# Performance work log

Hardware: AMD Instinct MI355X
Metric: run time of the kernel (lower is better)

Reference implementation:

```python
import jax, jax.numpy as jnp
import numpy as np

B, T, N = 16, 1000, 100
ENC, VOCAB, EMB, HID, ATT, PROJ = 512, 10025, 640, 1024, 1024, 1024


def setup_inputs() -> dict:
    key = jax.random.key(0)
    ks = jax.random.split(key, 20)
    g = lambda k, shape, s=0.02: (jax.random.normal(k, shape) * s).astype(jnp.float32)
    inp = {
        "encoder_outputs": jax.random.normal(ks[0], (B, T, ENC), dtype=jnp.float32),
        "labels": jax.random.randint(ks[1], (B, N), 0, VOCAB),
        "enc_seq_len": jax.random.randint(ks[2], (B,), T // 2, T + 1),
        # parameters (torch layout: Linear weight [out, in])
        "embed_table": g(ks[3], (VOCAB, EMB)),
        "W_ih": g(ks[4], (4 * HID, EMB + ENC)),
        "W_hh": g(ks[5], (4 * HID, HID)),
        "b_ih": jnp.zeros((4 * HID,), jnp.float32),
        "b_hh": jnp.zeros((4 * HID,), jnp.float32),
        "W_s": g(ks[6], (ATT, HID)),              # s_transformed, no bias
        "W_enc": g(ks[7], (ATT, ENC)),            # enc_ctx
        "b_enc": jnp.zeros((ATT,), jnp.float32),
        "v_att": g(ks[8], (ATT,)),                # attention energy vector
        "W_fert": g(ks[9], (ENC,)),               # inv_fertility [1,ENC] squeezed
        "W_fb": g(ks[10], (ATT,)),                # weight_feedback [ATT,1] squeezed
        "W_ro": g(ks[11], (PROJ, HID + EMB + ENC)),
        "b_ro": jnp.zeros((PROJ,), jnp.float32),
        "W_out": g(ks[12], (VOCAB, PROJ // 2)),
        "b_out": jnp.zeros((VOCAB,), jnp.float32),
    }
    return inp


def _decode(encoder_outputs, labels, enc_seq_len, embed_table, W_ih, W_hh, b_ih,
            b_hh, W_s, W_enc, b_enc, v_att, W_fert, W_fb, W_ro, b_ro, W_out, b_out):
    Bb, Tt, _ = encoder_outputs.shape
    # shifted target embeddings: pad one zero step at front, drop last -> [B,N,EMB]
    emb = embed_table[labels]
    emb = jnp.concatenate([jnp.zeros_like(emb[:, :1]), emb[:, :-1]], axis=1)

    enc_ctx = jnp.einsum("btd,ad->bta", encoder_outputs, W_enc) + b_enc  # [B,T,ATT]
    inv_fert = jax.nn.sigmoid(encoder_outputs @ W_fert)                   # [B,T]
    seq_mask = jnp.arange(Tt)[None, :] < enc_seq_len[:, None]             # [B,T]

    def step(carry, e_t):
        h, c, att_ctx, accum = carry  # h,c:[B,HID]  att_ctx:[B,ENC]  accum:[B,T]
        x = jnp.concatenate([e_t, att_ctx], axis=-1)
        gates = x @ W_ih.T + b_ih + h @ W_hh.T + b_hh
        i, f, gg, o = jnp.split(gates, 4, axis=-1)
        c_new = jax.nn.sigmoid(f) * c + jax.nn.sigmoid(i) * jnp.tanh(gg)
        h_new = jax.nn.sigmoid(o) * jnp.tanh(c_new)

        s_t = h_new @ W_s.T                                   # [B,ATT]
        wf = accum[:, :, None] * W_fb[None, None, :]          # [B,T,ATT]
        energies = jnp.tanh(enc_ctx + s_t[:, None, :] + wf) @ v_att  # [B,T]
        energies = jnp.where(seq_mask, energies, -jnp.inf)
        weights = jax.nn.softmax(energies, axis=1)            # [B,T]
        ctx = jnp.einsum("bt,btd->bd", weights, encoder_outputs)
        accum_new = accum + weights * inv_fert * 0.5
        return (h_new, c_new, ctx, accum_new), (h_new, ctx)

    carry0 = (
        jnp.zeros((Bb, HID), jnp.float32),
        jnp.zeros((Bb, HID), jnp.float32),
        jnp.zeros((Bb, ENC), jnp.float32),
        jnp.zeros((Bb, Tt), jnp.float32),
    )
    carry, (s_seq, ctx_seq) = jax.lax.scan(step, carry0, emb.transpose(1, 0, 2))
    s_stacked = s_seq.transpose(1, 0, 2)        # [B,N,HID]
    ctx_stacked = ctx_seq.transpose(1, 0, 2)    # [B,N,ENC]

    ro_in = jnp.concatenate([s_stacked, emb, ctx_stacked], axis=-1) @ W_ro.T + b_ro
    readout = jnp.max(ro_in.reshape(Bb, ro_in.shape[1], -1, 2), axis=-1)  # maxout
    logits = readout @ W_out.T + b_out
    return logits, carry


def reference(encoder_outputs, labels, enc_seq_len, embed_table, W_ih, W_hh, b_ih,
              b_hh, W_s, W_enc, b_enc, v_att, W_fert, W_fb, W_ro, b_ro, W_out, b_out):
    logits, (h, c, att_ctx, accum) = _decode(
        encoder_outputs, labels, enc_seq_len, embed_table, W_ih, W_hh, b_ih, b_hh,
        W_s, W_enc, b_enc, v_att, W_fert, W_fb, W_ro, b_ro, W_out, b_out)
    return logits, h, c, att_ctx, accum
```

## Files before the change

kernel.cpp:

```cpp
#include <hip/hip_runtime.h>
#include <math.h>

#define Bsz 16
#define Tsz 1000
#define Nsz 100
#define ENC 512
#define VOCAB 10025
#define EMB 640
#define HID 1024
#define ATT 1024
#define KX (EMB + ENC)
#define KRO (HID + EMB + ENC)
#define G4 (4 * HID)

typedef short s16x8 __attribute__((ext_vector_type(8)));
typedef unsigned short u16x4 __attribute__((ext_vector_type(4)));
typedef unsigned short u16x8 __attribute__((ext_vector_type(8)));
typedef float f32x4 __attribute__((ext_vector_type(4)));

__device__ __forceinline__ float4 ld4(const float* p) { return *reinterpret_cast<const float4*>(p); }
__device__ __forceinline__ float dot4(float4 a, float4 b) { return a.x*b.x + a.y*b.y + a.z*b.z + a.w*b.w; }
__device__ __forceinline__ float sigmoidf_(float x) { return 1.f / (1.f + __expf(-x)); }
__device__ __forceinline__ float ftanh_(float x) {
    x = fminf(15.f, fmaxf(-15.f, x));
    float e = __expf(2.f * x);
    return (e - 1.f) / (e + 1.f);
}
__device__ __forceinline__ unsigned short f2bf(float x) {
    union { float f; unsigned u; } v; v.f = x;
    unsigned r = v.u + 0x7fffu + ((v.u >> 16) & 1u);
    return (unsigned short)(r >> 16);
}
__device__ __forceinline__ float bf2f(unsigned short h) {
    union { float f; unsigned u; } v; v.u = ((unsigned)h) << 16;
    return v.f;
}

__global__ __launch_bounds__(256) void k_init(float* accum, const float* __restrict__ bih,
                                              const float* __restrict__ bhh, float* __restrict__ bsum) {
    int i = blockIdx.x * 256 + threadIdx.x;
    if (i < Bsz * Tsz) accum[i] = 0.f;
    if (i < G4) bsum[i] = bih[i] + bhh[i];
}

__global__ __launch_bounds__(256) void k_embed(const int* __restrict__ labels,
                                               const float* __restrict__ table,
                                               float* __restrict__ roA) {
    int idx = blockIdx.x * 256 + threadIdx.x;
    if (idx >= Bsz * Nsz * EMB) return;
    int e = idx % EMB;
    int bn = idx / EMB;
    int n = bn % Nsz, b = bn / Nsz;
    float v = 0.f;
    if (n > 0) {
        int lab = labels[b * Nsz + n - 1];
        v = table[(size_t)lab * EMB + e];
    }
    roA[(size_t)bn * KRO + HID + e] = v;
}

template <int MODE>
__global__ __launch_bounds__(256) void mfma_gemm(const float* __restrict__ A, int lda,
                                                 const float* __restrict__ W, int ldw,
                                                 const float* __restrict__ bias,
                                                 float* __restrict__ C,
                                                 int M, int Nc, int K, int ldC) {
    __shared__ unsigned short Ah[128][40], Al[128][40], Wh[128][40], Wl[128][40];
    int tid = threadIdx.x;
    int lane = tid & 63;
    int wave = tid >> 6;
    int wm = (wave >> 1) * 64, wn = (wave & 1) * 64;
    int m0 = blockIdx.y * 128, n0 = blockIdx.x * 128;
    int lrow = tid >> 1;
    int lcol = (tid & 1) * 16;
    bool aval = (m0 + lrow) < M;
    bool wval = (n0 + lrow) < Nc;
    const float* Arow = A + (size_t)(m0 + lrow) * lda + lcol;
    const float* Wrow = W + (size_t)(n0 + lrow) * ldw + lcol;
    int frow = lane & 15, fk = (lane >> 4) * 8;

    f32x4 acc[4][4];
#pragma unroll
    for (int i = 0; i < 4; i++)
#pragma unroll
        for (int j = 0; j < 4; j++) acc[i][j] = (f32x4){0.f, 0.f, 0.f, 0.f};

    const float4 z4 = {0.f, 0.f, 0.f, 0.f};
    for (int k0 = 0; k0 < K; k0 += 32) {
#pragma unroll
        for (int c = 0; c < 16; c += 4) {
            float4 av = aval ? ld4(Arow + k0 + c) : z4;
            u16x4 hv, lv;
            hv.x = f2bf(av.x); lv.x = f2bf(av.x - bf2f(hv.x));
            hv.y = f2bf(av.y); lv.y = f2bf(av.y - bf2f(hv.y));
            hv.z = f2bf(av.z); lv.z = f2bf(av.z - bf2f(hv.z));
            hv.w = f2bf(av.w); lv.w = f2bf(av.w - bf2f(hv.w));
            *(u16x4*)&Ah[lrow][lcol + c] = hv;
            *(u16x4*)&Al[lrow][lcol + c] = lv;
            float4 wv = wval ? ld4(Wrow + k0 + c) : z4;
            hv.x = f2bf(wv.x); lv.x = f2bf(wv.x - bf2f(hv.x));
            hv.y = f2bf(wv.y); lv.y = f2bf(wv.y - bf2f(hv.y));
            hv.z = f2bf(wv.z); lv.z = f2bf(wv.z - bf2f(hv.z));
            hv.w = f2bf(wv.w); lv.w = f2bf(wv.w - bf2f(hv.w));
            *(u16x4*)&Wh[lrow][lcol + c] = hv;
            *(u16x4*)&Wl[lrow][lcol + c] = lv;
        }
        __syncthreads();
        s16x8 afh[4], afl[4], bfh[4], bfl[4];
#pragma unroll
        for (int i = 0; i < 4; i++) {
            afh[i] = *(const s16x8*)&Ah[wm + i * 16 + frow][fk];
            afl[i] = *(const s16x8*)&Al[wm + i * 16 + frow][fk];
            bfh[i] = *(const s16x8*)&Wh[wn + i * 16 + frow][fk];
            bfl[i] = *(const s16x8*)&Wl[wn + i * 16 + frow][fk];
        }
#pragma unroll
        for (int mi = 0; mi < 4; mi++)
#pragma unroll
            for (int ni = 0; ni < 4; ni++) {
                acc[mi][ni] = __builtin_amdgcn_mfma_f32_16x16x32_bf16(afh[mi], bfh[ni], acc[mi][ni], 0, 0, 0);
                acc[mi][ni] = __builtin_amdgcn_mfma_f32_16x16x32_bf16(afl[mi], bfh[ni], acc[mi][ni], 0, 0, 0);
                acc[mi][ni] = __builtin_amdgcn_mfma_f32_16x16x32_bf16(afh[mi], bfl[ni], acc[mi][ni], 0, 0, 0);
            }
        __syncthreads();
    }
    int crb = (lane >> 4) * 4;
    int ccol = lane & 15;
#pragma unroll
    for (int mi = 0; mi < 4; mi++) {
#pragma unroll
        for (int r = 0; r < 4; r++) {
            int m = m0 + wm + mi * 16 + crb + r;
#pragma unroll
            for (int ni = 0; ni < 4; ni++) {
                int n = n0 + wn + ni * 16 + ccol;
                if (MODE == 0) {
                    if (m < M && n < Nc) C[(size_t)m * ldC + n] = acc[mi][ni][r] + bias[n];
                } else if (MODE == 2) {
                    if (m < M && n < Nc)
                        ((unsigned short*)C)[(size_t)m * ldC + n] = f2bf(acc[mi][ni][r] + bias[n]);
                } else {
                    float v = (n < Nc) ? acc[mi][ni][r] + bias[n] : -INFINITY;
                    float o = __shfl_xor(v, 1, 64);
                    if (((lane & 1) == 0) && m < M && n < Nc)
                        C[(size_t)m * ldC + (n >> 1)] = fmaxf(v, o);
                }
            }
        }
    }
}

__global__ __launch_bounds__(256) void k_ifert(const float* __restrict__ enc,
                                               const float* __restrict__ Wfert,
                                               float* __restrict__ ifert) {
    int wv = (blockIdx.x * 256 + threadIdx.x) >> 6;
    int lane = threadIdx.x & 63;
    if (wv >= Bsz * Tsz) return;
    const float* row = enc + (size_t)wv * ENC;
    float s = 0.f;
    for (int k = lane * 4; k < ENC; k += 256) s += dot4(ld4(row + k), ld4(Wfert + k));
    for (int o = 32; o; o >>= 1) s += __shfl_xor(s, o, 64);
    if (lane == 0) ifert[wv] = 1.f / (1.f + __expf(-s));
}

__global__ __launch_bounds__(256) void k_gates2(float* __restrict__ roA, float* __restrict__ cbuf,
                                                const float* __restrict__ gpre,
                                                const float* __restrict__ Wih, const float* __restrict__ Whh,
                                                int t) {
    __shared__ float red[4][4][16];
    int lane = threadIdx.x & 63;
    int wid = threadIdx.x >> 6;
    int j = blockIdx.x * 4 + wid;
    float acc[4][16];
#pragma unroll
    for (int g = 0; g < 4; g++)
#pragma unroll
        for (int b = 0; b < 16; b++) acc[g][b] = 0.f;
    if (t > 0) {
        const float* wc0 = Wih + (size_t)(0 * HID + j) * KX + EMB;
        const float* wc1 = Wih + (size_t)(1 * HID + j) * KX + EMB;
        const float* wc2 = Wih + (size_t)(2 * HID + j) * KX + EMB;
        const float* wc3 = Wih + (size_t)(3 * HID + j) * KX + EMB;
        const float* wh0 = Whh + (size_t)(0 * HID + j) * HID;
        const float* wh1 = Whh + (size_t)(1 * HID + j) * HID;
        const float* wh2 = Whh + (size_t)(2 * HID + j) * HID;
        const float* wh3 = Whh + (size_t)(3 * HID + j) * HID;
        for (int k = lane * 4; k < ENC; k += 256) {
            float4 w0 = ld4(wc0 + k), w1 = ld4(wc1 + k), w2 = ld4(wc2 + k), w3 = ld4(wc3 + k);
#pragma unroll
            for (int b = 0; b < 16; b++) {
                float4 x = ld4(&roA[(size_t)(b * Nsz + t - 1) * KRO + HID + EMB + k]);
                acc[0][b] += dot4(w0, x); acc[1][b] += dot4(w1, x);
                acc[2][b] += dot4(w2, x); acc[3][b] += dot4(w3, x);
            }
        }
        for (int k = lane * 4; k < HID; k += 256) {
            float4 w0 = ld4(wh0 + k), w1 = ld4(wh1 + k), w2 = ld4(wh2 + k), w3 = ld4(wh3 + k);
#pragma unroll
            for (int b = 0; b < 16; b++) {
                float4 x = ld4(&roA[(size_t)(b * Nsz + t - 1) * KRO + k]);
                acc[0][b] += dot4(w0, x); acc[1][b] += dot4(w1, x);
                acc[2][b] += dot4(w2, x); acc[3][b] += dot4(w3, x);
            }
        }
    }
#pragma unroll
    for (int g = 0; g < 4; g++)
#pragma unroll
        for (int b = 0; b < 16; b++) {
            float v = acc[g][b];
            for (int o = 32; o; o >>= 1) v += __shfl_xor(v, o, 64);
            if (lane == 0) red[wid][g][b] = v;
        }
    __syncthreads();
    if (lane < 16) {
        int b = lane;
        const float* gp = gpre + (size_t)(b * Nsz + t) * G4 + j;
        float gi = red[wid][0][b] + gp[0];
        float gf = red[wid][1][b] + gp[HID];
        float gg = red[wid][2][b] + gp[2 * HID];
        float go = red[wid][3][b] + gp[3 * HID];
        float cold = (t > 0) ? cbuf[b * HID + j] : 0.f;
        float cn = sigmoidf_(gf) * cold + sigmoidf_(gi) * ftanh_(gg);
        float hn = sigmoidf_(go) * ftanh_(cn);
        cbuf[b * HID + j] = cn;
        roA[(size_t)(b * Nsz + t) * KRO + j] = hn;
    }
}

__global__ __launch_bounds__(256) void k_s(const float* __restrict__ roA, const float* __restrict__ Wsm,
                                           float* __restrict__ st, int t) {
    int wv = (blockIdx.x * 256 + threadIdx.x) >> 6;
    int lane = threadIdx.x & 63;
    float acc[16];
#pragma unroll
    for (int b = 0; b < 16; b++) acc[b] = 0.f;
    const float* wr = Wsm + (size_t)wv * HID;
    for (int k = lane * 4; k < HID; k += 256) {
        float4 w = ld4(wr + k);
#pragma unroll
        for (int b = 0; b < 16; b++) acc[b] += dot4(w, ld4(&roA[(size_t)(b * Nsz + t) * KRO + k]));
    }
#pragma unroll
    for (int b = 0; b < 16; b++) {
        float v = acc[b];
        for (int o = 32; o; o >>= 1) v += __shfl_xor(v, o, 64);
        acc[b] = v;
    }
    if (lane < 16) st[lane * ATT + wv] = acc[lane];
}

__global__ __launch_bounds__(256) void k_energy(const unsigned short* __restrict__ encctx,
                                                const float* __restrict__ st,
                                                const float* __restrict__ Wfb,
                                                const float* __restrict__ vatt,
                                                const float* __restrict__ accum,
                                                const int* __restrict__ seqlen,
                                                float* __restrict__ enw,
                                                float* __restrict__ roA, int tstep) {
    if (blockIdx.x < Bsz) {
        float* dst = roA + (size_t)(blockIdx.x * Nsz + tstep) * KRO + HID + EMB;
        dst[threadIdx.x] = 0.f;
        dst[threadIdx.x + 256] = 0.f;
    }
    int wv = (blockIdx.x * 256 + threadIdx.x) >> 6;
    int lane = threadIdx.x & 63;
    int b = wv / Tsz, t = wv - b * Tsz;
    if (t >= seqlen[b]) {
        if (lane == 0) enw[wv] = -INFINITY;
        return;
    }
    float ac = accum[wv];
    const unsigned short* ec = encctx + (size_t)wv * ATT;
    const float* sr = st + b * ATT;
    float e = 0.f;
    for (int k = lane * 8; k < ATT; k += 512) {
        u16x8 c8 = *(const u16x8*)(ec + k);
        float4 sa = ld4(sr + k), sb = ld4(sr + k + 4);
        float4 fa = ld4(Wfb + k), fb = ld4(Wfb + k + 4);
        float4 va = ld4(vatt + k), vb = ld4(vatt + k + 4);
        e += ftanh_(bf2f(c8[0]) + sa.x + ac * fa.x) * va.x;
        e += ftanh_(bf2f(c8[1]) + sa.y + ac * fa.y) * va.y;
        e += ftanh_(bf2f(c8[2]) + sa.z + ac * fa.z) * va.z;
        e += ftanh_(bf2f(c8[3]) + sa.w + ac * fa.w) * va.w;
        e += ftanh_(bf2f(c8[4]) + sb.x + ac * fb.x) * vb.x;
        e += ftanh_(bf2f(c8[5]) + sb.y + ac * fb.y) * vb.y;
        e += ftanh_(bf2f(c8[6]) + sb.z + ac * fb.z) * vb.z;
        e += ftanh_(bf2f(c8[7]) + sb.w + ac * fb.w) * vb.w;
    }
    for (int o = 32; o; o >>= 1) e += __shfl_xor(e, o, 64);
    if (lane == 0) enw[wv] = e;
}

#define TCH 10
__global__ __launch_bounds__(256) void k_softctx(const float* __restrict__ enw,
                                                 const float* __restrict__ ifert,
                                                 float* __restrict__ accum,
                                                 const float* __restrict__ enc,
                                                 const int* __restrict__ seqlen,
                                                 float* __restrict__ roA, int tstep) {
    int b = blockIdx.y, tid = threadIdx.x;
    __shared__ float redm[4], reds[4];
    int len = seqlen[b];
    const float* row = enw + b * Tsz;
    float m = -INFINITY;
    for (int i = tid; i < len; i += 256) m = fmaxf(m, row[i]);
    for (int o = 32; o; o >>= 1) m = fmaxf(m, __shfl_xor(m, o, 64));
    if ((tid & 63) == 0) redm[tid >> 6] = m;
    __syncthreads();
    float M = fmaxf(fmaxf(redm[0], redm[1]), fmaxf(redm[2], redm[3]));
    float s = 0.f;
    for (int i = tid; i < len; i += 256) s += __expf(row[i] - M);
    for (int o = 32; o; o >>= 1) s += __shfl_xor(s, o, 64);
    if ((tid & 63) == 0) reds[tid >> 6] = s;
    __syncthreads();
    float inv = 1.f / (reds[0] + reds[1] + reds[2] + reds[3]);
    int t0 = blockIdx.x * (Tsz / TCH);
    int t1 = min(t0 + Tsz / TCH, len);
    for (int i = t0 + tid; i < t1; i += 256)
        accum[b * Tsz + i] += __expf(row[i] - M) * inv * ifert[b * Tsz + i] * 0.5f;
    if (t0 >= t1) return;
    float a0 = 0.f, a1 = 0.f;
    for (int i = t0; i < t1; i++) {
        float w = __expf(row[i] - M) * inv;
        const float* er = enc + (size_t)(b * Tsz + i) * ENC;
        a0 += w * er[tid];
        a1 += w * er[tid + 256];
    }
    float* dst = roA + (size_t)(b * Nsz + tstep) * KRO + HID + EMB;
    atomicAdd(dst + tid, a0);
    atomicAdd(dst + tid + 256, a1);
}

__global__ __launch_bounds__(256) void k_final(const float* __restrict__ roA, const float* __restrict__ cbuf,
                                               const float* __restrict__ accum, float* __restrict__ out) {
    int idx = blockIdx.x * 256 + threadIdx.x;
    const int base = Bsz * Nsz * VOCAB;
    const int OH = Bsz * HID, OC = Bsz * HID, OA = Bsz * ENC, OAC = Bsz * Tsz;
    if (idx < OH) {
        int b = idx / HID, j = idx % HID;
        out[base + idx] = roA[(size_t)(b * Nsz + Nsz - 1) * KRO + j];
        return;
    }
    idx -= OH;
    if (idx < OC) { out[base + OH + idx] = cbuf[idx]; return; }
    idx -= OC;
    if (idx < OA) {
        int b = idx / ENC, d = idx % ENC;
        out[base + OH + OC + idx] = roA[(size_t)(b * Nsz + Nsz - 1) * KRO + HID + EMB + d];
        return;
    }
    idx -= OA;
    if (idx < OAC) out[base + OH + OC + OA + idx] = accum[idx];
}

extern "C" void kernel_launch(void* const* d_in, const int* in_sizes, int n_in,
                              void* d_out, int out_size, void* d_ws, size_t ws_size,
                              hipStream_t stream) {
    const float* enc   = (const float*)d_in[0];
    const int* labels  = (const int*)d_in[1];
    const int* seqlen  = (const int*)d_in[2];
    const float* table = (const float*)d_in[3];
    const float* Wih   = (const float*)d_in[4];
    const float* Whh   = (const float*)d_in[5];
    const float* bih   = (const float*)d_in[6];
    const float* bhh   = (const float*)d_in[7];
    const float* Wsm   = (const float*)d_in[8];
    const float* Wenc  = (const float*)d_in[9];
    const float* benc  = (const float*)d_in[10];
    const float* vatt  = (const float*)d_in[11];
    const float* Wfert = (const float*)d_in[12];
    const float* Wfb   = (const float*)d_in[13];
    const float* Wro   = (const float*)d_in[14];
    const float* bro   = (const float*)d_in[15];
    const float* Wout  = (const float*)d_in[16];
    const float* bout  = (const float*)d_in[17];
    float* out = (float*)d_out;

    float* ws = (float*)d_ws;
    float* roA  = ws;
    float* cbuf = roA + (size_t)1600 * KRO;
    float* gpre = cbuf + Bsz * HID;
    unsigned short* encctx = (unsigned short*)(gpre + (size_t)1600 * G4);
    float* after = gpre + (size_t)1600 * G4 + (size_t)Bsz * Tsz * ATT / 2;
    float* ifert = after;
    float* accum = ifert + Bsz * Tsz;
    float* enw   = accum + Bsz * Tsz;
    float* st    = enw + Bsz * Tsz;
    float* bsum  = st + Bsz * ATT;
    float* rmx   = bsum + G4;

    k_init<<<(Bsz * Tsz + 255) / 256, 256, 0, stream>>>(accum, bih, bhh, bsum);
    k_embed<<<(Bsz * Nsz * EMB + 255) / 256, 256, 0, stream>>>(labels, table, roA);
    mfma_gemm<0><<<dim3(G4 / 128, (1600 + 127) / 128), 256, 0, stream>>>(
        roA + HID, KRO, Wih, KX, bsum, gpre, 1600, G4, EMB, G4);
    mfma_gemm<2><<<dim3(ATT / 128, (Bsz * Tsz) / 128), 256, 0, stream>>>(
        enc, ENC, Wenc, ENC, benc, (float*)encctx, Bsz * Tsz, ATT, ENC, ATT);
    k_ifert<<<(Bsz * Tsz * 64 + 255) / 256, 256, 0, stream>>>(enc, Wfert, ifert);

    for (int t = 0; t < Nsz; t++) {
        k_gates2<<<256, 256, 0, stream>>>(roA, cbuf, gpre, Wih, Whh, t);
        k_s<<<256, 256, 0, stream>>>(roA, Wsm, st, t);
        k_energy<<<(Bsz * Tsz * 64) / 256, 256, 0, stream>>>(encctx, st, Wfb, vatt, accum, seqlen,
                                                             enw, roA, t);
        k_softctx<<<dim3(TCH, Bsz), 256, 0, stream>>>(enw, ifert, accum, enc, seqlen, roA, t);
    }

    mfma_gemm<1><<<dim3(1024 / 128, (1600 + 127) / 128), 256, 0, stream>>>(
        roA, KRO, Wro, KRO, bro, rmx, 1600, 1024, KRO, 512);
    mfma_gemm<0><<<dim3((VOCAB + 127) / 128, (1600 + 127) / 128), 256, 0, stream>>>(
        rmx, 512, Wout, 512, bout, out, 1600, VOCAB, 512, VOCAB);
    k_final<<<(Bsz * HID * 2 + Bsz * ENC + Bsz * Tsz + 255) / 256, 256, 0, stream>>>(roA, cbuf, accum, out);
}
```

Baseline: 9.156 ms.

## Fuse decoder time loop into one persistent kernel with grid barriers

Replaces the 400 per-step kernel launches (gates, s-projection, energy, softmax/context) with a single persistent 256-block kernel that loops over all 100 steps, using atomic-counter grid barriers between phases. LSTM gate weights and W_s rows are cached in shared memory once per block instead of being re-read from global memory each step. Softmax drops the max-subtraction and uses a global sum of exponentials gathered through per-block partials, and the tanh clamp is removed. The cost is spin-wait barriers that assume all 256 blocks are co-resident, and possible overflow in the unstabilised exp and tanh.

```diff
diff --git a/kernel.cpp b/kernel.cpp
--- a/kernel.cpp
+++ b/kernel.cpp
@@ -22,9 +22,8 @@
 __device__ __forceinline__ float dot4(float4 a, float4 b) { return a.x*b.x + a.y*b.y + a.z*b.z + a.w*b.w; }
 __device__ __forceinline__ float sigmoidf_(float x) { return 1.f / (1.f + __expf(-x)); }
 __device__ __forceinline__ float ftanh_(float x) {
-    x = fminf(15.f, fmaxf(-15.f, x));
     float e = __expf(2.f * x);
-    return (e - 1.f) / (e + 1.f);
+    return 1.f - 2.f / (e + 1.f);
 }
 __device__ __forceinline__ unsigned short f2bf(float x) {
     union { float f; unsigned u; } v; v.f = x;
@@ -36,11 +35,24 @@
     return v.f;
 }
 
+__device__ __forceinline__ void gsync(unsigned* ctr, unsigned target) {
+    __threadfence();
+    __syncthreads();
+    if (threadIdx.x == 0) {
+        __hip_atomic_fetch_add(ctr, 1u, __ATOMIC_ACQ_REL, __HIP_MEMORY_SCOPE_AGENT);
+        while (__hip_atomic_load(ctr, __ATOMIC_ACQUIRE, __HIP_MEMORY_SCOPE_AGENT) < target)
+            __builtin_amdgcn_s_sleep(2);
+    }
+    __syncthreads();
+}
+
 __global__ __launch_bounds__(256) void k_init(float* accum, const float* __restrict__ bih,
-                                              const float* __restrict__ bhh, float* __restrict__ bsum) {
+                                              const float* __restrict__ bhh, float* __restrict__ bsum,
+                                              unsigned* bar) {
     int i = blockIdx.x * 256 + threadIdx.x;
     if (i < Bsz * Tsz) accum[i] = 0.f;
     if (i < G4) bsum[i] = bih[i] + bhh[i];
+    if (i == 0) *bar = 0u;
 }
 
 __global__ __launch_bounds__(256) void k_embed(const int* __restrict__ labels,
@@ -163,173 +175,193 @@
     if (lane == 0) ifert[wv] = 1.f / (1.f + __expf(-s));
 }
 
-__global__ __launch_bounds__(256) void k_gates2(float* __restrict__ roA, float* __restrict__ cbuf,
-                                                const float* __restrict__ gpre,
-                                                const float* __restrict__ Wih, const float* __restrict__ Whh,
-                                                int t) {
-    __shared__ float red[4][4][16];
-    int lane = threadIdx.x & 63;
-    int wid = threadIdx.x >> 6;
-    int j = blockIdx.x * 4 + wid;
-    float acc[4][16];
-#pragma unroll
-    for (int g = 0; g < 4; g++)
-#pragma unroll
-        for (int b = 0; b < 16; b++) acc[g][b] = 0.f;
-    if (t > 0) {
-        const float* wc0 = Wih + (size_t)(0 * HID + j) * KX + EMB;
-        const float* wc1 = Wih + (size_t)(1 * HID + j) * KX + EMB;
-        const float* wc2 = Wih + (size_t)(2 * HID + j) * KX + EMB;
-        const float* wc3 = Wih + (size_t)(3 * HID + j) * KX + EMB;
-        const float* wh0 = Whh + (size_t)(0 * HID + j) * HID;
-        const float* wh1 = Whh + (size_t)(1 * HID + j) * HID;
-        const float* wh2 = Whh + (size_t)(2 * HID + j) * HID;
-        const float* wh3 = Whh + (size_t)(3 * HID + j) * HID;
-        for (int k = lane * 4; k < ENC; k += 256) {
-            float4 w0 = ld4(wc0 + k), w1 = ld4(wc1 + k), w2 = ld4(wc2 + k), w3 = ld4(wc3 + k);
-#pragma unroll
-            for (int b = 0; b < 16; b++) {
-                float4 x = ld4(&roA[(size_t)(b * Nsz + t - 1) * KRO + HID + EMB + k]);
-                acc[0][b] += dot4(w0, x); acc[1][b] += dot4(w1, x);
-                acc[2][b] += dot4(w2, x); acc[3][b] += dot4(w3, x);
-            }
-        }
-        for (int k = lane * 4; k < HID; k += 256) {
-            float4 w0 = ld4(wh0 + k), w1 = ld4(wh1 + k), w2 = ld4(wh2 + k), w3 = ld4(wh3 + k);
-#pragma unroll
-            for (int b = 0; b < 16; b++) {
-                float4 x = ld4(&roA[(size_t)(b * Nsz + t - 1) * KRO + k]);
-                acc[0][b] += dot4(w0, x); acc[1][b] += dot4(w1, x);
-                acc[2][b] += dot4(w2, x); acc[3][b] += dot4(w3, x);
-            }
-        }
-    }
-#pragma unroll
-    for (int g = 0; g < 4; g++)
-#pragma unroll
-        for (int b = 0; b < 16; b++) {
-            float v = acc[g][b];
-            for (int o = 32; o; o >>= 1) v += __shfl_xor(v, o, 64);
-            if (lane == 0) red[wid][g][b] = v;
-        }
+__global__ __launch_bounds__(256, 1) void k_scan(
+    float* __restrict__ roA, float* __restrict__ cbuf,
+    const float* __restrict__ gpre, const unsigned short* __restrict__ encctx,
+    const float* __restrict__ ifert, float* __restrict__ accum,
+    float* __restrict__ enw, float* __restrict__ st, float* __restrict__ pexp,
+    const float* __restrict__ enc, const int* __restrict__ seqlen,
+    const float* __restrict__ Wih, const float* __restrict__ Whh,
+    const float* __restrict__ Wsm, const float* __restrict__ Wfb,
+    const float* __restrict__ vatt, unsigned* bar) {
+    __shared__ float Wg[16][1540];
+    __shared__ float Ws4[4][1028];
+    __shared__ float redbuf[16];
+    const int p = blockIdx.x, tid = threadIdx.x;
+    const int lane = tid & 63, jj = tid >> 6;
+    const int bg = lane >> 4, ks4 = (lane & 15) << 2;
+    const bool ks0 = (lane & 15) == 0;
+    const int j = 4 * p + jj;
+
+    for (int r = 0; r < 16; r++) {
+        int g = r & 3, j2 = 4 * p + (r >> 2);
+        const float* s1 = Wih + (size_t)(g * HID + j2) * KX + EMB;
+        const float* s2 = Whh + (size_t)(g * HID + j2) * HID;
+        for (int k = tid * 4; k < 512; k += 1024) *(float4*)&Wg[r][k] = ld4(s1 + k);
+        for (int k = tid * 4; k < 1024; k += 1024) *(float4*)&Wg[r][512 + k] = ld4(s2 + k);
+    }
+    for (int r = 0; r < 4; r++) {
+        const float* s = Wsm + (size_t)(4 * p + r) * HID;
+        for (int k = tid * 4; k < 1024; k += 1024) *(float4*)&Ws4[r][k] = ld4(s + k);
+    }
     __syncthreads();
-    if (lane < 16) {
-        int b = lane;
-        const float* gp = gpre + (size_t)(b * Nsz + t) * G4 + j;
-        float gi = red[wid][0][b] + gp[0];
-        float gf = red[wid][1][b] + gp[HID];
-        float gg = red[wid][2][b] + gp[2 * HID];
-        float go = red[wid][3][b] + gp[3 * HID];
-        float cold = (t > 0) ? cbuf[b * HID + j] : 0.f;
-        float cn = sigmoidf_(gf) * cold + sigmoidf_(gi) * ftanh_(gg);
-        float hn = sigmoidf_(go) * ftanh_(cn);
-        cbuf[b * HID + j] = cn;
-        roA[(size_t)(b * Nsz + t) * KRO + j] = hn;
-    }
-}
-
-__global__ __launch_bounds__(256) void k_s(const float* __restrict__ roA, const float* __restrict__ Wsm,
-                                           float* __restrict__ st, int t) {
-    int wv = (blockIdx.x * 256 + threadIdx.x) >> 6;
-    int lane = threadIdx.x & 63;
-    float acc[16];
-#pragma unroll
-    for (int b = 0; b < 16; b++) acc[b] = 0.f;
-    const float* wr = Wsm + (size_t)wv * HID;
-    for (int k = lane * 4; k < HID; k += 256) {
-        float4 w = ld4(wr + k);
-#pragma unroll
-        for (int b = 0; b < 16; b++) acc[b] += dot4(w, ld4(&roA[(size_t)(b * Nsz + t) * KRO + k]));
-    }
-#pragma unroll
-    for (int b = 0; b < 16; b++) {
-        float v = acc[b];
-        for (int o = 32; o; o >>= 1) v += __shfl_xor(v, o, 64);
-        acc[b] = v;
-    }
-    if (lane < 16) st[lane * ATT + wv] = acc[lane];
-}
-
-__global__ __launch_bounds__(256) void k_energy(const unsigned short* __restrict__ encctx,
-                                                const float* __restrict__ st,
-                                                const float* __restrict__ Wfb,
-                                                const float* __restrict__ vatt,
-                                                const float* __restrict__ accum,
-                                                const int* __restrict__ seqlen,
-                                                float* __restrict__ enw,
-                                                float* __restrict__ roA, int tstep) {
-    if (blockIdx.x < Bsz) {
-        float* dst = roA + (size_t)(blockIdx.x * Nsz + tstep) * KRO + HID + EMB;
-        dst[threadIdx.x] = 0.f;
-        dst[threadIdx.x + 256] = 0.f;
-    }
-    int wv = (blockIdx.x * 256 + threadIdx.x) >> 6;
-    int lane = threadIdx.x & 63;
-    int b = wv / Tsz, t = wv - b * Tsz;
-    if (t >= seqlen[b]) {
-        if (lane == 0) enw[wv] = -INFINITY;
-        return;
-    }
-    float ac = accum[wv];
-    const unsigned short* ec = encctx + (size_t)wv * ATT;
-    const float* sr = st + b * ATT;
-    float e = 0.f;
-    for (int k = lane * 8; k < ATT; k += 512) {
-        u16x8 c8 = *(const u16x8*)(ec + k);
-        float4 sa = ld4(sr + k), sb = ld4(sr + k + 4);
-        float4 fa = ld4(Wfb + k), fb = ld4(Wfb + k + 4);
-        float4 va = ld4(vatt + k), vb = ld4(vatt + k + 4);
-        e += ftanh_(bf2f(c8[0]) + sa.x + ac * fa.x) * va.x;
-        e += ftanh_(bf2f(c8[1]) + sa.y + ac * fa.y) * va.y;
-        e += ftanh_(bf2f(c8[2]) + sa.z + ac * fa.z) * va.z;
-        e += ftanh_(bf2f(c8[3]) + sa.w + ac * fa.w) * va.w;
-        e += ftanh_(bf2f(c8[4]) + sb.x + ac * fb.x) * vb.x;
-        e += ftanh_(bf2f(c8[5]) + sb.y + ac * fb.y) * vb.y;
-        e += ftanh_(bf2f(c8[6]) + sb.z + ac * fb.z) * vb.z;
-        e += ftanh_(bf2f(c8[7]) + sb.w + ac * fb.w) * vb.w;
-    }
-    for (int o = 32; o; o >>= 1) e += __shfl_xor(e, o, 64);
-    if (lane == 0) enw[wv] = e;
-}
-
-#define TCH 10
-__global__ __launch_bounds__(256) void k_softctx(const float* __restrict__ enw,
-                                                 const float* __restrict__ ifert,
-                                                 float* __restrict__ accum,
-                                                 const float* __restrict__ enc,
-                                                 const int* __restrict__ seqlen,
-                                                 float* __restrict__ roA, int tstep) {
-    int b = blockIdx.y, tid = threadIdx.x;
-    __shared__ float redm[4], reds[4];
-    int len = seqlen[b];
-    const float* row = enw + b * Tsz;
-    float m = -INFINITY;
-    for (int i = tid; i < len; i += 256) m = fmaxf(m, row[i]);
-    for (int o = 32; o; o >>= 1) m = fmaxf(m, __shfl_xor(m, o, 64));
-    if ((tid & 63) == 0) redm[tid >> 6] = m;
-    __syncthreads();
-    float M = fmaxf(fmaxf(redm[0], redm[1]), fmaxf(redm[2], redm[3]));
-    float s = 0.f;
-    for (int i = tid; i < len; i += 256) s += __expf(row[i] - M);
-    for (int o = 32; o; o >>= 1) s += __shfl_xor(s, o, 64);
-    if ((tid & 63) == 0) reds[tid >> 6] = s;
-    __syncthreads();
-    float inv = 1.f / (reds[0] + reds[1] + reds[2] + reds[3]);
-    int t0 = blockIdx.x * (Tsz / TCH);
-    int t1 = min(t0 + Tsz / TCH, len);
-    for (int i = t0 + tid; i < t1; i += 256)
-        accum[b * Tsz + i] += __expf(row[i] - M) * inv * ifert[b * Tsz + i] * 0.5f;
-    if (t0 >= t1) return;
-    float a0 = 0.f, a1 = 0.f;
-    for (int i = t0; i < t1; i++) {
-        float w = __expf(row[i] - M) * inv;
-        const float* er = enc + (size_t)(b * Tsz + i) * ENC;
-        a0 += w * er[tid];
-        a1 += w * er[tid + 256];
-    }
-    float* dst = roA + (size_t)(b * Nsz + tstep) * KRO + HID + EMB;
-    atomicAdd(dst + tid, a0);
-    atomicAdd(dst + tid + 256, a1);
+
+    unsigned barcnt = 0;
+    for (int t = 0; t < Nsz; t++) {
+        float acc[4][4];
+#pragma unroll
+        for (int g = 0; g < 4; g++)
+#pragma unroll
+            for (int bb = 0; bb < 4; bb++) acc[g][bb] = 0.f;
+        if (t > 0) {
+            const float* xr[4];
+#pragma unroll
+            for (int bb = 0; bb < 4; bb++)
+                xr[bb] = roA + ((size_t)((4 * bg + bb) * Nsz + (t - 1))) * KRO;
+            const int r0 = jj * 4;
+            for (int c = 0; c < 8; c++) {
+                int k = c * 64 + ks4;
+                float4 w0 = *(const float4*)&Wg[r0][k];
+                float4 w1 = *(const float4*)&Wg[r0 + 1][k];
+                float4 w2 = *(const float4*)&Wg[r0 + 2][k];
+                float4 w3 = *(const float4*)&Wg[r0 + 3][k];
+#pragma unroll
+                for (int bb = 0; bb < 4; bb++) {
+                    float4 x = ld4(xr[bb] + (HID + EMB) + k);
+                    acc[0][bb] += dot4(w0, x); acc[1][bb] += dot4(w1, x);
+                    acc[2][bb] += dot4(w2, x); acc[3][bb] += dot4(w3, x);
+                }
+            }
+            for (int c = 0; c < 16; c++) {
+                int k = 512 + c * 64 + ks4;
+                float4 w0 = *(const float4*)&Wg[r0][k];
+                float4 w1 = *(const float4*)&Wg[r0 + 1][k];
+                float4 w2 = *(const float4*)&Wg[r0 + 2][k];
+                float4 w3 = *(const float4*)&Wg[r0 + 3][k];
+#pragma unroll
+                for (int bb = 0; bb < 4; bb++) {
+                    float4 x = ld4(xr[bb] + (k - 512));
+                    acc[0][bb] += dot4(w0, x); acc[1][bb] += dot4(w1, x);
+                    acc[2][bb] += dot4(w2, x); acc[3][bb] += dot4(w3, x);
+                }
+            }
+#pragma unroll
+            for (int g = 0; g < 4; g++)
+#pragma unroll
+                for (int bb = 0; bb < 4; bb++) {
+                    float v = acc[g][bb];
+                    v += __shfl_xor(v, 1, 64); v += __shfl_xor(v, 2, 64);
+                    v += __shfl_xor(v, 4, 64); v += __shfl_xor(v, 8, 64);
+                    acc[g][bb] = v;
+                }
+        }
+        if (ks0) {
+#pragma unroll
+            for (int bb = 0; bb < 4; bb++) {
+                int b = 4 * bg + bb;
+                const float* gp = gpre + ((size_t)(b * Nsz + t)) * G4 + j;
+                float gi = acc[0][bb] + gp[0];
+                float gf = acc[1][bb] + gp[HID];
+                float gg = acc[2][bb] + gp[2 * HID];
+                float go = acc[3][bb] + gp[3 * HID];
+                float cold = (t > 0) ? cbuf[b * HID + j] : 0.f;
+                float cn = sigmoidf_(gf) * cold + sigmoidf_(gi) * ftanh_(gg);
+                float hn = sigmoidf_(go) * ftanh_(cn);
+                cbuf[b * HID + j] = cn;
+                roA[((size_t)(b * Nsz + t)) * KRO + j] = hn;
+            }
+        }
+        barcnt++; gsync(bar, barcnt * 256u);
+
+        {
+            float sa[4] = {0.f, 0.f, 0.f, 0.f};
+            for (int c = 0; c < 16; c++) {
+                int k = c * 64 + ks4;
+                float4 w = *(const float4*)&Ws4[jj][k];
+#pragma unroll
+                for (int bb = 0; bb < 4; bb++) {
+                    float4 x = ld4(roA + ((size_t)((4 * bg + bb) * Nsz + t)) * KRO + k);
+                    sa[bb] += dot4(w, x);
+                }
+            }
+#pragma unroll
+            for (int bb = 0; bb < 4; bb++) {
+                float v = sa[bb];
+                v += __shfl_xor(v, 1, 64); v += __shfl_xor(v, 2, 64);
+                v += __shfl_xor(v, 4, 64); v += __shfl_xor(v, 8, 64);
+                if (ks0) st[(4 * bg + bb) * ATT + j] = v;
+            }
+            if (p < Bsz) {
+                float* dst = roA + ((size_t)(p * Nsz + t)) * KRO + HID + EMB;
+                dst[tid] = 0.f;
+                dst[tid + 256] = 0.f;
+            }
+        }
+        barcnt++; gsync(bar, barcnt * 256u);
+
+        if (tid < 16) redbuf[tid] = 0.f;
+        __syncthreads();
+        for (int pair = p * 4 + jj; pair < Bsz * Tsz; pair += 1024) {
+            int b = pair / Tsz, tt = pair - b * Tsz;
+            float ew = 0.f;
+            if (tt < seqlen[b]) {
+                float ac = accum[pair];
+                float e = 0.f;
+#pragma unroll
+                for (int it = 0; it < 2; it++) {
+                    int k = lane * 8 + it * 512;
+                    u16x8 c8 = *(const u16x8*)(encctx + (size_t)pair * ATT + k);
+                    float4 s1 = ld4(st + b * ATT + k), s2 = ld4(st + b * ATT + k + 4);
+                    float4 f1 = ld4(Wfb + k), f2 = ld4(Wfb + k + 4);
+                    float4 v1 = ld4(vatt + k), v2 = ld4(vatt + k + 4);
+                    e += ftanh_(bf2f(c8[0]) + s1.x + ac * f1.x) * v1.x;
+                    e += ftanh_(bf2f(c8[1]) + s1.y + ac * f1.y) * v1.y;
+                    e += ftanh_(bf2f(c8[2]) + s1.z + ac * f1.z) * v1.z;
+                    e += ftanh_(bf2f(c8[3]) + s1.w + ac * f1.w) * v1.w;
+                    e += ftanh_(bf2f(c8[4]) + s2.x + ac * f2.x) * v2.x;
+                    e += ftanh_(bf2f(c8[5]) + s2.y + ac * f2.y) * v2.y;
+                    e += ftanh_(bf2f(c8[6]) + s2.z + ac * f2.z) * v2.z;
+                    e += ftanh_(bf2f(c8[7]) + s2.w + ac * f2.w) * v2.w;
+                }
+                for (int o = 32; o; o >>= 1) e += __shfl_xor(e, o, 64);
+                ew = __expf(e);
+            }
+            if (lane == 0) {
+                enw[pair] = ew;
+                if (ew > 0.f) atomicAdd(&redbuf[b], ew);
+            }
+        }
+        __syncthreads();
+        if (tid < 16) pexp[p * 16 + tid] = redbuf[tid];
+        barcnt++; gsync(bar, barcnt * 256u);
+
+        {
+            int b = p >> 4, chunk = p & 15;
+            float ps = pexp[tid * 16 + b];
+            for (int o = 32; o; o >>= 1) ps += __shfl_xor(ps, o, 64);
+            if (lane == 0) redbuf[jj] = ps;
+            __syncthreads();
+            float inv = 1.f / (redbuf[0] + redbuf[1] + redbuf[2] + redbuf[3]);
+            int len = seqlen[b];
+            int t0 = chunk * 63, t1 = min(t0 + 63, len);
+            if (t0 < t1) {
+                const float* row = enw + b * Tsz;
+                for (int i = t0 + tid; i < t1; i += 256)
+                    accum[b * Tsz + i] += row[i] * inv * ifert[b * Tsz + i] * 0.5f;
+                float a0 = 0.f, a1 = 0.f;
+                for (int i = t0; i < t1; i++) {
+                    float w = row[i] * inv;
+                    const float* er = enc + ((size_t)(b * Tsz + i)) * ENC;
+                    a0 += w * er[tid];
+                    a1 += w * er[tid + 256];
+                }
+                float* dst = roA + ((size_t)(b * Nsz + t)) * KRO + HID + EMB;
+                atomicAdd(dst + tid, a0);
+                atomicAdd(dst + tid + 256, a1);
+            }
+        }
+        barcnt++; gsync(bar, barcnt * 256u);
+    }
 }
 
 __global__ __launch_bounds__(256) void k_final(const float* __restrict__ roA, const float* __restrict__ cbuf,
@@ -382,15 +414,16 @@
     float* cbuf = roA + (size_t)1600 * KRO;
     float* gpre = cbuf + Bsz * HID;
     unsigned short* encctx = (unsigned short*)(gpre + (size_t)1600 * G4);
-    float* after = gpre + (size_t)1600 * G4 + (size_t)Bsz * Tsz * ATT / 2;
-    float* ifert = after;
+    float* ifert = gpre + (size_t)1600 * G4 + (size_t)Bsz * Tsz * ATT / 2;
     float* accum = ifert + Bsz * Tsz;
     float* enw   = accum + Bsz * Tsz;
     float* st    = enw + Bsz * Tsz;
     float* bsum  = st + Bsz * ATT;
-    float* rmx   = bsum + G4;
-
-    k_init<<<(Bsz * Tsz + 255) / 256, 256, 0, stream>>>(accum, bih, bhh, bsum);
+    float* pexp  = bsum + G4;
+    unsigned* bar = (unsigned*)(pexp + 4096);
+    float* rmx   = pexp + 4096 + 16;
+
+    k_init<<<(Bsz * Tsz + 255) / 256, 256, 0, stream>>>(accum, bih, bhh, bsum, bar);
     k_embed<<<(Bsz * Nsz * EMB + 255) / 256, 256, 0, stream>>>(labels, table, roA);
     mfma_gemm<0><<<dim3(G4 / 128, (1600 + 127) / 128), 256, 0, stream>>>(
         roA + HID, KRO, Wih, KX, bsum, gpre, 1600, G4, EMB, G4);
@@ -398,13 +431,8 @@
         enc, ENC, Wenc, ENC, benc, (float*)encctx, Bsz * Tsz, ATT, ENC, ATT);
     k_ifert<<<(Bsz * Tsz * 64 + 255) / 256, 256, 0, stream>>>(enc, Wfert, ifert);
 
-    for (int t = 0; t < Nsz; t++) {
-        k_gates2<<<256, 256, 0, stream>>>(roA, cbuf, gpre, Wih, Whh, t);
-        k_s<<<256, 256, 0, stream>>>(roA, Wsm, st, t);
-        k_energy<<<(Bsz * Tsz * 64) / 256, 256, 0, stream>>>(encctx, st, Wfb, vatt, accum, seqlen,
-                                                             enw, roA, t);
-        k_softctx<<<dim3(TCH, Bsz), 256, 0, stream>>>(enw, ifert, accum, enc, seqlen, roA, t);
-    }
+    k_scan<<<256, 256, 0, stream>>>(roA, cbuf, gpre, encctx, ifert, accum, enw, st, pexp,
+                                    enc, seqlen, Wih, Whh, Wsm, Wfb, vatt, bar);
 
     mfma_gemm<1><<<dim3(1024 / 128, (1600 + 127) / 128), 256, 0, stream>>>(
         roA, KRO, Wro, KRO, bro, rmx, 1600, 1024, KRO, 512);
```

Result: slower. 23.58 ms (+157.6%).
